# Kernel optimization log

Measured on AMD Instinct MI355X. Metric: run time of the kernel, lower is better.

Reference implementation:

```python
import jax, jax.numpy as jnp
import numpy as np

ALPHA = 1.0


def setup_inputs() -> dict:
    key = jax.random.key(0)
    ks = jax.random.split(key, 7)
    B, S, D_IN, D_OUT, R = 4, 2048, 2048, 2048, 64
    return {
        "x": jax.random.normal(ks[0], (B, S, D_IN), dtype=jnp.float32),
        "weight": jax.random.normal(ks[1], (D_OUT, D_IN), dtype=jnp.float32) * 0.02,
        "bias": jax.random.normal(ks[2], (D_OUT,), dtype=jnp.float32) * 0.02,
        "U": jax.random.normal(ks[3], (D_OUT, R), dtype=jnp.float32) * 0.02,
        "sigma": jax.random.normal(ks[4], (R, R), dtype=jnp.float32) * 0.02,
        "R": jax.random.normal(ks[5], (R, R), dtype=jnp.float32) * 0.02,
        "Vt": jax.random.normal(ks[6], (R, D_IN), dtype=jnp.float32) * 0.02,
    }


def reference(x, weight, bias, U, sigma, R, Vt):
    # base linear: F.linear(x, W, b) = x @ W^T + b
    base_out = jnp.einsum("bsi,oi->bso", x, weight) + bias
    # LoRA-XS delta: alpha * U @ sigma @ R @ Vt  -> [d_out, d_in]
    delta_W = ALPHA * (U @ sigma @ R @ Vt)
    lora_out = jnp.einsum("bsi,oi->bso", x, delta_W)
    return base_out + lora_out
```

## Files before the change

kernel.cpp:

```cpp
#include <hip/hip_runtime.h>
#include <hip/hip_bf16.h>
#include <stdint.h>

#define M_DIM 8192
#define K_DIM 2048
#define N_DIM 2048
#define RANK  64
#define ALPHA_F 1.0f

typedef __attribute__((ext_vector_type(4))) float  f32x4;
typedef __attribute__((ext_vector_type(8))) short  s16x8;

__device__ __forceinline__ unsigned short f2bf(float f) {
    unsigned int u = __float_as_uint(f);
    u += 0x7fffu + ((u >> 16) & 1u);
    return (unsigned short)(u >> 16);
}

__device__ __forceinline__ void gload_lds16(const void* g, void* l) {
    __builtin_amdgcn_global_load_lds(
        (const __attribute__((address_space(1))) void*)g,
        (__attribute__((address_space(3))) void*)l, 16, 0, 0);
}


__global__ __launch_bounds__(256) void t2sr_kernel(const float* __restrict__ sigma,
                                                   const float* __restrict__ Rm,
                                                   const float* __restrict__ Vt,
                                                   float* __restrict__ T2) {
    __shared__ float sSig[64];
    __shared__ float sRow[64];
    const int r = blockIdx.x >> 3;
    const int i = (blockIdx.x & 7) * 256 + threadIdx.x;
    if (threadIdx.x < 64) sSig[threadIdx.x] = sigma[r * 64 + threadIdx.x];
    __syncthreads();
    if (threadIdx.x < 64) {
        float a = 0.f;
        #pragma unroll 8
        for (int k = 0; k < 64; ++k) a += sSig[k] * Rm[k * 64 + threadIdx.x];
        sRow[threadIdx.x] = a;
    }
    __syncthreads();
    float a = 0.f;
    #pragma unroll 8
    for (int k = 0; k < 64; ++k) a += sRow[k] * Vt[k * 2048 + i];
    T2[r * 2048 + i] = a;
}

__global__ __launch_bounds__(256) void weffcast_kernel(const float* __restrict__ W,
                                                       const float* __restrict__ U,
                                                       const float* __restrict__ T2,
                                                       unsigned short* __restrict__ Wb,
                                                       const float* __restrict__ x,
                                                       unsigned short* __restrict__ xb) {
    __shared__ float sU[64 * 65];
    __shared__ float sT[64 * 64];
    if (blockIdx.x < 1024) {
        int to = blockIdx.x >> 5;
        int ti = blockIdx.x & 31;
        int o0 = to * 64, i0 = ti * 64;
        for (int e = 0; e < 16; ++e) {
            int li = threadIdx.x + e * 256;
            int hi = li >> 6, lo = li & 63;
            sU[hi * 65 + lo] = U[(size_t)o0 * 64 + li];
            sT[li]           = T2[hi * 2048 + i0 + lo];
        }
        __syncthreads();
        int o  = threadIdx.x >> 2;
        int ib = (threadIdx.x & 3) * 16;
        float acc[16] = {};
        for (int k = 0; k < 64; ++k) {
            float u = sU[o * 65 + k];
            #pragma unroll
            for (int j = 0; j < 16; ++j) acc[j] += u * sT[k * 64 + ib + j];
        }
        size_t base = (size_t)(o0 + o) * 2048 + i0 + ib;
        #pragma unroll
        for (int j = 0; j < 16; ++j)
            Wb[base + j] = f2bf(W[base + j] + ALPHA_F * acc[j]);
    } else {
        int cb = blockIdx.x - 1024;
        #pragma unroll
        for (int rep = 0; rep < 4; ++rep) {
            size_t idx = (((size_t)cb * 4 + rep) * 256 + threadIdx.x) * 8;
            f32x4 a = *reinterpret_cast<const f32x4*>(x + idx);
            f32x4 b = *reinterpret_cast<const f32x4*>(x + idx + 4);
            s16x8 o;
            o[0] = (short)f2bf(a[0]); o[1] = (short)f2bf(a[1]);
            o[2] = (short)f2bf(a[2]); o[3] = (short)f2bf(a[3]);
            o[4] = (short)f2bf(b[0]); o[5] = (short)f2bf(b[1]);
            o[6] = (short)f2bf(b[2]); o[7] = (short)f2bf(b[3]);
            *reinterpret_cast<s16x8*>(xb + idx) = o;
        }
    }
}


#define AHALF_E (128 * K_DIM)

__device__ __forceinline__ void stage_slot(const unsigned short* g0, const unsigned short* g1,
                                           char* smp, int ldsbase, int wave) {
    gload_lds16(g0, smp + ldsbase + wave * 1024);
    gload_lds16(g1, smp + ldsbase + 8192 + wave * 1024);
}

template <int B_, int P_>
__device__ __forceinline__ void read_a4(const char* sm, s16x8 (&af)[4], int wr8, int laneoff) {
    constexpr int ks = P_ & 1, mh = P_ >> 1;
    #pragma unroll
    for (int mi = 0; mi < 4; ++mi)
        af[mi] = *(const s16x8*)(sm + B_ * 32768 +
                    ((wr8 + mh * 4 + mi) * 2 + ks) * 1024 + laneoff);
}

template <int B_, int P_>
__device__ __forceinline__ void read_b4(const char* sm, s16x8 (&bfr4)[4][2], int wc4, int laneoff) {
    constexpr int ks = P_ & 1;
    #pragma unroll
    for (int ni = 0; ni < 4; ++ni)
        bfr4[ni][ks] = *(const s16x8*)(sm + 65536 + B_ * 32768 +
                          ((wc4 + ni) * 2 + ks) * 1024 + laneoff);
}

template <int P_>
__device__ __forceinline__ void mfma_p(f32x4 (&acc)[8][4], s16x8 (&af)[4], s16x8 (&bfr4)[4][2]) {
    constexpr int ks = P_ & 1, mh = P_ >> 1;
    #pragma unroll
    for (int mi = 0; mi < 4; ++mi)
        #pragma unroll
        for (int ni = 0; ni < 4; ++ni)
            acc[mh * 4 + mi][ni] = __builtin_amdgcn_mfma_f32_16x16x32_bf16(
                af[mi], bfr4[ni][ks], acc[mh * 4 + mi][ni], 0, 0, 0);
}

#define VMWAIT2 do { asm volatile("s_waitcnt vmcnt(2)" ::: "memory"); \
                     __builtin_amdgcn_sched_barrier(0); } while (0)
#define VMWAIT4 do { asm volatile("s_waitcnt vmcnt(4)" ::: "memory"); \
                     __builtin_amdgcn_sched_barrier(0); } while (0)

#define DO_PHASE(B_, P_, STAGE_STMT, WAIT_STMT)                         \
  { s16x8 af[4];                                                        \
    read_a4<B_, P_>(sm, af, wr8, laneoff);                              \
    if (P_ < 2) read_b4<B_, P_>(sm, bfr4, wc4, laneoff);                \
    STAGE_STMT;                                                         \
    WAIT_STMT;                                                          \
    __builtin_amdgcn_s_barrier();                                       \
    asm volatile("s_waitcnt lgkmcnt(0)" ::: "memory");                  \
    __builtin_amdgcn_sched_barrier(0);                                  \
    __builtin_amdgcn_s_setprio(1);                                      \
    mfma_p<P_>(acc, af, bfr4);                                          \
    __builtin_amdgcn_s_setprio(0); }

#define STAGE_A(half, buf, kel) \
    stage_slot(Ag + (half) * AHALF_E + (kel) + soff0, Ag + (half) * AHALF_E + (kel) + soff1, \
               sm, (buf) * 32768 + (half) * 16384, wave)
#define STAGE_B(half, buf, kel) \
    stage_slot(Bg + (half) * AHALF_E + (kel) + soff0, Bg + (half) * AHALF_E + (kel) + soff1, \
               sm, 65536 + (buf) * 32768 + (half) * 16384, wave)

__global__ __launch_bounds__(512, 2)
void gemm8_kernel(const unsigned short* __restrict__ A,
                  const unsigned short* __restrict__ Bm,
                  const float* __restrict__ bias,
                  float* __restrict__ C) {
    extern __shared__ char sm[];

    const int tid  = threadIdx.x;
    const int wave = tid >> 6;
    const int lane = tid & 63;
    const int wr8  = (wave >> 2) * 8;
    const int wc4  = (wave & 3) * 4;

    const int bid = blockIdx.x;
    const int swz = (bid & 7) * 32 + (bid >> 3);
    const int rowM0 = (swz >> 3) * 256;
    const int rowN0 = (swz & 7) * 256;

    const unsigned short* Ag = A  + (size_t)rowM0 * K_DIM;
    const unsigned short* Bg = Bm + (size_t)rowN0 * K_DIM;

    int soff0, soff1;
    {
        #pragma unroll
        for (int ld = 0; ld < 2; ++ld) {
            int D   = ld * 8192 + tid * 16;
            int st  = D >> 10;
            int s   = (D >> 4) & 63;
            int row = s >> 2;
            int kq  = (s & 3) ^ ((s >> 3) & 3);
            int e = ((st >> 1) * 16 + row) * K_DIM + (st & 1) * 32 + kq * 8;
            if (ld == 0) soff0 = e; else soff1 = e;
        }
    }

    const int laneoff = ((lane & 15) * 4 + ((lane >> 4) ^ (((lane & 15) >> 1) & 3))) * 16;

    f32x4 acc[8][4] = {};
    s16x8 bfr4[4][2];

    STAGE_A(0, 0, 0);
    STAGE_A(1, 0, 0);
    STAGE_B(0, 0, 0);
    STAGE_B(1, 0, 0);
    STAGE_B(0, 1, 64);
    STAGE_B(1, 1, 64);
    VMWAIT4;
    __builtin_amdgcn_s_barrier();

    for (int i = 0; i < 16; ++i) {
        const int kA12 = (2 * i + 1) * 64;
        const int kN2  = ((2 * i + 2) & 31) * 64;
        const int kN3  = ((2 * i + 3) & 31) * 64;

        DO_PHASE(0, 0, STAGE_A(0, 1, kA12), ((void)0));
        DO_PHASE(0, 1, STAGE_A(1, 1, kA12), ((void)0));
        DO_PHASE(0, 2, ((void)0),           ((void)0));
        DO_PHASE(0, 3, STAGE_B(0, 0, kN2),  VMWAIT2);
        DO_PHASE(1, 0, STAGE_B(1, 0, kN2),  ((void)0));
        DO_PHASE(1, 1, STAGE_A(0, 0, kN2),  ((void)0));
        DO_PHASE(1, 2, STAGE_A(1, 0, kN2),  ((void)0));
        DO_PHASE(1, 3, (STAGE_B(0, 1, kN3), STAGE_B(1, 1, kN3)), VMWAIT4);
    }

    const int col0  = rowN0 + (wc4 >> 2) * 64 + (lane & 15);
    const int row0w = rowM0 + (wr8 >> 3) * 128 + (lane >> 4) * 4;
    float bv[4];
    #pragma unroll
    for (int ni = 0; ni < 4; ++ni) bv[ni] = bias[col0 + ni * 16];
    #pragma unroll
    for (int mi = 0; mi < 8; ++mi)
        #pragma unroll
        for (int ni = 0; ni < 4; ++ni)
            #pragma unroll
            for (int r = 0; r < 4; ++r)
                C[(size_t)(row0w + mi * 16 + r) * N_DIM + col0 + ni * 16] =
                    acc[mi][ni][r] + bv[ni];
}


__global__ __launch_bounds__(256) void xt_kernel(const float* __restrict__ x,
                                                 const float* __restrict__ T2,
                                                 float* __restrict__ xt) {
    int idx = blockIdx.x * 256 + threadIdx.x;
    int m = idx >> 6, r = idx & 63;
    float acc = 0.f;
    for (int i = 0; i < K_DIM; ++i) acc += x[(size_t)m * K_DIM + i] * T2[r * K_DIM + i];
    xt[idx] = acc;
}

__global__ __launch_bounds__(256) void fgemm_kernel(const float* __restrict__ A,
                                                    const float* __restrict__ W,
                                                    const float* __restrict__ xt,
                                                    const float* __restrict__ U,
                                                    const float* __restrict__ bias,
                                                    float* __restrict__ C) {
    __shared__ float sA[64][17];
    __shared__ float sW[64][17];
    int bm = blockIdx.x >> 5;
    int bn = blockIdx.x & 31;
    int m0 = bm * 64, n0 = bn * 64;
    int tid = threadIdx.x;
    int tm = tid >> 4, tn = tid & 15;
    float acc[4][4] = {};
    for (int k0 = 0; k0 < K_DIM; k0 += 16) {
        int lr = tid >> 2;
        int lc = (tid & 3) * 4;
        #pragma unroll
        for (int j = 0; j < 4; ++j) {
            sA[lr][lc + j] = A[(size_t)(m0 + lr) * K_DIM + k0 + lc + j];
            sW[lr][lc + j] = W[(size_t)(n0 + lr) * K_DIM + k0 + lc + j];
        }
        __syncthreads();
        #pragma unroll
        for (int kk = 0; kk < 16; ++kk) {
            float av[4], wv[4];
            #pragma unroll
            for (int i = 0; i < 4; ++i) av[i] = sA[tm * 4 + i][kk];
            #pragma unroll
            for (int j = 0; j < 4; ++j) wv[j] = sW[tn * 4 + j][kk];
            #pragma unroll
            for (int i = 0; i < 4; ++i)
                #pragma unroll
                for (int j = 0; j < 4; ++j) acc[i][j] += av[i] * wv[j];
        }
        __syncthreads();
    }
    #pragma unroll
    for (int i = 0; i < 4; ++i) {
        int m = m0 + tm * 4 + i;
        #pragma unroll
        for (int j = 0; j < 4; ++j) {
            int n = n0 + tn * 4 + j;
            float l = 0.f;
            for (int r = 0; r < RANK; ++r) l += xt[(size_t)m * RANK + r] * U[(size_t)n * RANK + r];
            C[(size_t)m * N_DIM + n] = acc[i][j] + l + bias[n];
        }
    }
}

extern "C" void kernel_launch(void* const* d_in, const int* in_sizes, int n_in,
                              void* d_out, int out_size, void* d_ws, size_t ws_size,
                              hipStream_t stream) {
    const float* x      = (const float*)d_in[0];
    const float* weight = (const float*)d_in[1];
    const float* bias   = (const float*)d_in[2];
    const float* U      = (const float*)d_in[3];
    const float* sigma  = (const float*)d_in[4];
    const float* Rm     = (const float*)d_in[5];
    const float* Vt     = (const float*)d_in[6];
    float* out = (float*)d_out;
    char* ws = (char*)d_ws;

    const size_t XB_BYTES = (size_t)M_DIM * K_DIM * 2;
    const size_t WB_BYTES = (size_t)N_DIM * K_DIM * 2;
    const size_t T2_BYTES = (size_t)RANK * K_DIM * 4;
    const size_t MAIN_NEED = XB_BYTES + WB_BYTES + T2_BYTES;

    if (ws_size >= MAIN_NEED) {
        unsigned short* xb = (unsigned short*)ws;
        unsigned short* wb = (unsigned short*)(ws + XB_BYTES);
        float* T2 = (float*)(ws + XB_BYTES + WB_BYTES);

        hipFuncSetAttribute((const void*)gemm8_kernel,
                            hipFuncAttributeMaxDynamicSharedMemorySize, 131072);

        t2sr_kernel<<<512, 256, 0, stream>>>(sigma, Rm, Vt, T2);
        weffcast_kernel<<<3072, 256, 0, stream>>>(weight, U, T2, wb, x, xb);
        gemm8_kernel<<<(M_DIM / 256) * (N_DIM / 256), 512, 131072, stream>>>(xb, wb, bias, out);
    } else {
        float* T2 = (float*)ws;
        float* xt = (float*)(ws + T2_BYTES);
        t2sr_kernel<<<512, 256, 0, stream>>>(sigma, Rm, Vt, T2);
        xt_kernel<<<(M_DIM * RANK) / 256, 256, 0, stream>>>(x, T2, xt);
        fgemm_kernel<<<(M_DIM / 64) * (N_DIM / 64), 256, 0, stream>>>(x, weight, xt, U, bias, out);
    }
}
```

Before: 93.78 us.

## Software-pipeline LDS fragment reads ahead of MFMA with double-buffered A fragments

```diff
diff --git a/kernel.cpp b/kernel.cpp
--- a/kernel.cpp
+++ b/kernel.cpp
@@ -138,17 +138,15 @@
 #define VMWAIT4 do { asm volatile("s_waitcnt vmcnt(4)" ::: "memory"); \
                      __builtin_amdgcn_sched_barrier(0); } while (0)
 
-#define DO_PHASE(B_, P_, STAGE_STMT, WAIT_STMT)                         \
-  { s16x8 af[4];                                                        \
-    read_a4<B_, P_>(sm, af, wr8, laneoff);                              \
-    if (P_ < 2) read_b4<B_, P_>(sm, bfr4, wc4, laneoff);                \
-    STAGE_STMT;                                                         \
+#define DO_PHASE(P_CONSUME_B, P_CONSUME_P, AFC, NEXTREAD_STMT, NWAIT_LIT, STAGE_STMT, WAIT_STMT) \
+  { STAGE_STMT;                                                         \
     WAIT_STMT;                                                          \
     __builtin_amdgcn_s_barrier();                                       \
-    asm volatile("s_waitcnt lgkmcnt(0)" ::: "memory");                  \
+    NEXTREAD_STMT;                                                      \
+    asm volatile("s_waitcnt lgkmcnt(" NWAIT_LIT ")" ::: "memory");      \
     __builtin_amdgcn_sched_barrier(0);                                  \
     __builtin_amdgcn_s_setprio(1);                                      \
-    mfma_p<P_>(acc, af, bfr4);                                          \
+    mfma_p<P_CONSUME_P>(acc, AFC, bfr4);                                \
     __builtin_amdgcn_s_setprio(0); }
 
 #define STAGE_A(half, buf, kel) \
@@ -196,6 +194,7 @@
     const int laneoff = ((lane & 15) * 4 + ((lane >> 4) ^ (((lane & 15) >> 1) & 3))) * 16;
 
     f32x4 acc[8][4] = {};
+    s16x8 afA[4], afB[4];
     s16x8 bfr4[4][2];
 
     STAGE_A(0, 0, 0);
@@ -206,20 +205,42 @@
     STAGE_B(1, 1, 64);
     VMWAIT4;
     __builtin_amdgcn_s_barrier();
+    read_a4<0, 0>(sm, afA, wr8, laneoff);
+    read_b4<0, 0>(sm, bfr4, wc4, laneoff);
 
     for (int i = 0; i < 16; ++i) {
         const int kA12 = (2 * i + 1) * 64;
         const int kN2  = ((2 * i + 2) & 31) * 64;
         const int kN3  = ((2 * i + 3) & 31) * 64;
 
-        DO_PHASE(0, 0, STAGE_A(0, 1, kA12), ((void)0));
-        DO_PHASE(0, 1, STAGE_A(1, 1, kA12), ((void)0));
-        DO_PHASE(0, 2, ((void)0),           ((void)0));
-        DO_PHASE(0, 3, STAGE_B(0, 0, kN2),  VMWAIT2);
-        DO_PHASE(1, 0, STAGE_B(1, 0, kN2),  ((void)0));
-        DO_PHASE(1, 1, STAGE_A(0, 0, kN2),  ((void)0));
-        DO_PHASE(1, 2, STAGE_A(1, 0, kN2),  ((void)0));
-        DO_PHASE(1, 3, (STAGE_B(0, 1, kN3), STAGE_B(1, 1, kN3)), VMWAIT4);
+        DO_PHASE(0, 0, afA,
+                 (read_a4<0, 1>(sm, afB, wr8, laneoff),
+                  read_b4<0, 1>(sm, bfr4, wc4, laneoff)), "8",
+                 STAGE_A(0, 1, kA12), ((void)0));
+        DO_PHASE(0, 1, afB,
+                 (read_a4<0, 2>(sm, afA, wr8, laneoff)), "4",
+                 STAGE_A(1, 1, kA12), ((void)0));
+        DO_PHASE(0, 2, afA,
+                 (read_a4<0, 3>(sm, afB, wr8, laneoff)), "4",
+                 ((void)0), ((void)0));
+        DO_PHASE(0, 3, afB,
+                 (read_a4<1, 0>(sm, afA, wr8, laneoff),
+                  read_b4<1, 0>(sm, bfr4, wc4, laneoff)), "8",
+                 STAGE_B(0, 0, kN2), VMWAIT2);
+        DO_PHASE(1, 0, afA,
+                 (read_a4<1, 1>(sm, afB, wr8, laneoff),
+                  read_b4<1, 1>(sm, bfr4, wc4, laneoff)), "8",
+                 STAGE_B(1, 0, kN2), ((void)0));
+        DO_PHASE(1, 1, afB,
+                 (read_a4<1, 2>(sm, afA, wr8, laneoff)), "4",
+                 STAGE_A(0, 0, kN2), ((void)0));
+        DO_PHASE(1, 2, afA,
+                 (read_a4<1, 3>(sm, afB, wr8, laneoff)), "4",
+                 STAGE_A(1, 0, kN2), ((void)0));
+        DO_PHASE(1, 3, afB,
+                 (read_a4<0, 0>(sm, afA, wr8, laneoff),
+                  read_b4<0, 0>(sm, bfr4, wc4, laneoff)), "8",
+                 (STAGE_B(0, 1, kN3), STAGE_B(1, 1, kN3)), VMWAIT4);
     }
 
     const int col0  = rowN0 + (wc4 >> 2) * 64 + (lane & 15);
```

New measurement: 94.87 us. No clear change (+1.2%).

## Retile GEMM to 256x128 blocks with 4 waves and triple-buffered K=32 stages

Applied to the files above, without the earlier changes.

```diff
diff --git a/kernel.cpp b/kernel.cpp
--- a/kernel.cpp
+++ b/kernel.cpp
@@ -96,69 +96,93 @@
 }
 
 
-#define AHALF_E (128 * K_DIM)
-
-__device__ __forceinline__ void stage_slot(const unsigned short* g0, const unsigned short* g1,
-                                           char* smp, int ldsbase, int wave) {
-    gload_lds16(g0, smp + ldsbase + wave * 1024);
-    gload_lds16(g1, smp + ldsbase + 8192 + wave * 1024);
-}
-
-template <int B_, int P_>
-__device__ __forceinline__ void read_a4(const char* sm, s16x8 (&af)[4], int wr8, int laneoff) {
-    constexpr int ks = P_ & 1, mh = P_ >> 1;
+#define BUF0 0
+#define BUF1 24576
+#define BUF2 49152
+
+__device__ __forceinline__ void stage_a(const unsigned short* Ag, int kel, char* sm,
+                                        int tgt, int wave, int soff) {
+    #pragma unroll
+    for (int j = 0; j < 4; ++j) {
+        int s = wave * 4 + j;
+        gload_lds16(Ag + kel + s * 32768 + soff, sm + tgt + s * 1024);
+    }
+}
+__device__ __forceinline__ void stage_b(const unsigned short* Bg, int kel, char* sm,
+                                        int tgt, int wave, int soff) {
+    #pragma unroll
+    for (int j = 0; j < 2; ++j) {
+        int s = wave * 2 + j;
+        gload_lds16(Bg + kel + s * 32768 + soff, sm + tgt + 16384 + s * 1024);
+    }
+}
+
+template <int MH>
+__device__ __forceinline__ void read_a4(const char* sm, int cbuf, s16x8 (&af)[4],
+                                        int wrA8, int laneoff) {
     #pragma unroll
     for (int mi = 0; mi < 4; ++mi)
-        af[mi] = *(const s16x8*)(sm + B_ * 32768 +
-                    ((wr8 + mh * 4 + mi) * 2 + ks) * 1024 + laneoff);
-}
-
-template <int B_, int P_>
-__device__ __forceinline__ void read_b4(const char* sm, s16x8 (&bfr4)[4][2], int wc4, int laneoff) {
-    constexpr int ks = P_ & 1;
+        af[mi] = *(const s16x8*)(sm + cbuf + (wrA8 + MH * 4 + mi) * 1024 + laneoff);
+}
+__device__ __forceinline__ void read_b4(const char* sm, int cbuf, s16x8 (&bfr)[4],
+                                        int wcB4, int laneoff) {
     #pragma unroll
     for (int ni = 0; ni < 4; ++ni)
-        bfr4[ni][ks] = *(const s16x8*)(sm + 65536 + B_ * 32768 +
-                          ((wc4 + ni) * 2 + ks) * 1024 + laneoff);
-}
-
-template <int P_>
-__device__ __forceinline__ void mfma_p(f32x4 (&acc)[8][4], s16x8 (&af)[4], s16x8 (&bfr4)[4][2]) {
-    constexpr int ks = P_ & 1, mh = P_ >> 1;
+        bfr[ni] = *(const s16x8*)(sm + cbuf + 16384 + (wcB4 + ni) * 1024 + laneoff);
+}
+
+template <int MH>
+__device__ __forceinline__ void mfma16(f32x4 (&acc)[8][4], s16x8 (&af)[4], s16x8 (&bfr)[4]) {
     #pragma unroll
     for (int mi = 0; mi < 4; ++mi)
         #pragma unroll
         for (int ni = 0; ni < 4; ++ni)
-            acc[mh * 4 + mi][ni] = __builtin_amdgcn_mfma_f32_16x16x32_bf16(
-                af[mi], bfr4[ni][ks], acc[mh * 4 + mi][ni], 0, 0, 0);
-}
-
-#define VMWAIT2 do { asm volatile("s_waitcnt vmcnt(2)" ::: "memory"); \
+            acc[MH * 4 + mi][ni] = __builtin_amdgcn_mfma_f32_16x16x32_bf16(
+                af[mi], bfr[ni], acc[MH * 4 + mi][ni], 0, 0, 0);
+}
+
+#define VMWAIT6 do { asm volatile("s_waitcnt vmcnt(6)" ::: "memory"); \
                      __builtin_amdgcn_sched_barrier(0); } while (0)
-#define VMWAIT4 do { asm volatile("s_waitcnt vmcnt(4)" ::: "memory"); \
-                     __builtin_amdgcn_sched_barrier(0); } while (0)
-
-#define DO_PHASE(B_, P_, STAGE_STMT, WAIT_STMT)                         \
-  { s16x8 af[4];                                                        \
-    read_a4<B_, P_>(sm, af, wr8, laneoff);                              \
-    if (P_ < 2) read_b4<B_, P_>(sm, bfr4, wc4, laneoff);                \
-    STAGE_STMT;                                                         \
-    WAIT_STMT;                                                          \
-    __builtin_amdgcn_s_barrier();                                       \
-    asm volatile("s_waitcnt lgkmcnt(0)" ::: "memory");                  \
-    __builtin_amdgcn_sched_barrier(0);                                  \
-    __builtin_amdgcn_s_setprio(1);                                      \
-    mfma_p<P_>(acc, af, bfr4);                                          \
+
+#define PH_TAIL                                                  \
+    __builtin_amdgcn_s_barrier();                                \
+    asm volatile("s_waitcnt lgkmcnt(0)" ::: "memory");           \
+    __builtin_amdgcn_sched_barrier(0);                           \
+    __builtin_amdgcn_s_setprio(1);
+
+#define PHA(CBUF, TBUF, KEL)                                     \
+  { s16x8 af[4];                                                 \
+    read_a4<0>(sm, CBUF, af, wrA8, laneoff);                     \
+    read_b4(sm, CBUF, bfr, wcB4, laneoff);                       \
+    stage_a(Ag, (KEL), sm, TBUF, wave, soff);                    \
+    PH_TAIL                                                      \
+    mfma16<0>(acc, af, bfr);                                     \
     __builtin_amdgcn_s_setprio(0); }
 
-#define STAGE_A(half, buf, kel) \
-    stage_slot(Ag + (half) * AHALF_E + (kel) + soff0, Ag + (half) * AHALF_E + (kel) + soff1, \
-               sm, (buf) * 32768 + (half) * 16384, wave)
-#define STAGE_B(half, buf, kel) \
-    stage_slot(Bg + (half) * AHALF_E + (kel) + soff0, Bg + (half) * AHALF_E + (kel) + soff1, \
-               sm, 65536 + (buf) * 32768 + (half) * 16384, wave)
-
-__global__ __launch_bounds__(512, 2)
+#define PHB(CBUF, TBUF, KEL)                                     \
+  { s16x8 af[4];                                                 \
+    read_a4<1>(sm, CBUF, af, wrA8, laneoff);                     \
+    stage_b(Bg, (KEL), sm, TBUF, wave, soff);                    \
+    VMWAIT6;                                                     \
+    PH_TAIL                                                      \
+    mfma16<1>(acc, af, bfr);                                     \
+    __builtin_amdgcn_s_setprio(0); }
+
+#define PHA_NS(CBUF)                                             \
+  { s16x8 af[4];                                                 \
+    read_a4<0>(sm, CBUF, af, wrA8, laneoff);                     \
+    read_b4(sm, CBUF, bfr, wcB4, laneoff);                       \
+    PH_TAIL                                                      \
+    mfma16<0>(acc, af, bfr);                                     \
+    __builtin_amdgcn_s_setprio(0); }
+#define PHB_NS(CBUF)                                             \
+  { s16x8 af[4];                                                 \
+    read_a4<1>(sm, CBUF, af, wrA8, laneoff);                     \
+    PH_TAIL                                                      \
+    mfma16<1>(acc, af, bfr);                                     \
+    __builtin_amdgcn_s_setprio(0); }
+
+__global__ __launch_bounds__(256, 2)
 void gemm8_kernel(const unsigned short* __restrict__ A,
                   const unsigned short* __restrict__ Bm,
                   const float* __restrict__ bias,
@@ -168,62 +192,46 @@
     const int tid  = threadIdx.x;
     const int wave = tid >> 6;
     const int lane = tid & 63;
-    const int wr8  = (wave >> 2) * 8;
-    const int wc4  = (wave & 3) * 4;
+    const int wrA8 = (wave >> 1) * 8;
+    const int wcB4 = (wave & 1) * 4;
 
     const int bid = blockIdx.x;
-    const int swz = (bid & 7) * 32 + (bid >> 3);
-    const int rowM0 = (swz >> 3) * 256;
-    const int rowN0 = (swz & 7) * 256;
+    const int swz = (bid & 7) * 64 + (bid >> 3);
+    const int rowM0 = (swz >> 4) * 256;
+    const int rowN0 = (swz & 15) * 128;
 
     const unsigned short* Ag = A  + (size_t)rowM0 * K_DIM;
     const unsigned short* Bg = Bm + (size_t)rowN0 * K_DIM;
 
-    int soff0, soff1;
-    {
-        #pragma unroll
-        for (int ld = 0; ld < 2; ++ld) {
-            int D   = ld * 8192 + tid * 16;
-            int st  = D >> 10;
-            int s   = (D >> 4) & 63;
-            int row = s >> 2;
-            int kq  = (s & 3) ^ ((s >> 3) & 3);
-            int e = ((st >> 1) * 16 + row) * K_DIM + (st & 1) * 32 + kq * 8;
-            if (ld == 0) soff0 = e; else soff1 = e;
-        }
-    }
+    const int soff = (lane >> 2) * K_DIM + ((lane & 3) ^ ((lane >> 3) & 3)) * 8;
 
     const int laneoff = ((lane & 15) * 4 + ((lane >> 4) ^ (((lane & 15) >> 1) & 3))) * 16;
 
     f32x4 acc[8][4] = {};
-    s16x8 bfr4[4][2];
-
-    STAGE_A(0, 0, 0);
-    STAGE_A(1, 0, 0);
-    STAGE_B(0, 0, 0);
-    STAGE_B(1, 0, 0);
-    STAGE_B(0, 1, 64);
-    STAGE_B(1, 1, 64);
-    VMWAIT4;
+    s16x8 bfr[4];
+
+    stage_a(Ag, 0, sm, BUF0, wave, soff);
+    stage_b(Bg, 0, sm, BUF0, wave, soff);
+    stage_a(Ag, 32, sm, BUF1, wave, soff);
+    stage_b(Bg, 32, sm, BUF1, wave, soff);
+    VMWAIT6;
     __builtin_amdgcn_s_barrier();
 
-    for (int i = 0; i < 16; ++i) {
-        const int kA12 = (2 * i + 1) * 64;
-        const int kN2  = ((2 * i + 2) & 31) * 64;
-        const int kN3  = ((2 * i + 3) & 31) * 64;
-
-        DO_PHASE(0, 0, STAGE_A(0, 1, kA12), ((void)0));
-        DO_PHASE(0, 1, STAGE_A(1, 1, kA12), ((void)0));
-        DO_PHASE(0, 2, ((void)0),           ((void)0));
-        DO_PHASE(0, 3, STAGE_B(0, 0, kN2),  VMWAIT2);
-        DO_PHASE(1, 0, STAGE_B(1, 0, kN2),  ((void)0));
-        DO_PHASE(1, 1, STAGE_A(0, 0, kN2),  ((void)0));
-        DO_PHASE(1, 2, STAGE_A(1, 0, kN2),  ((void)0));
-        DO_PHASE(1, 3, (STAGE_B(0, 1, kN3), STAGE_B(1, 1, kN3)), VMWAIT4);
-    }
-
-    const int col0  = rowN0 + (wc4 >> 2) * 64 + (lane & 15);
-    const int row0w = rowM0 + (wr8 >> 3) * 128 + (lane >> 4) * 4;
+    for (int i = 0; i < 21; ++i) {
+        const int k2 = (3 * i + 2) * 32;
+        const int k3 = (3 * i + 3) * 32;
+        const int k4 = ((3 * i + 4) & 63) * 32;
+
+        PHA(BUF0, BUF2, k2); PHB(BUF0, BUF2, k2);
+        PHA(BUF1, BUF0, k3); PHB(BUF1, BUF0, k3);
+        PHA(BUF2, BUF1, k4); PHB(BUF2, BUF1, k4);
+    }
+    PHA_NS(BUF0); PHB_NS(BUF0);
+
+    asm volatile("s_waitcnt vmcnt(0)" ::: "memory");
+
+    const int col0  = rowN0 + (wave & 1) * 64 + (lane & 15);
+    const int row0w = rowM0 + (wave >> 1) * 128 + (lane >> 4) * 4;
     float bv[4];
     #pragma unroll
     for (int ni = 0; ni < 4; ++ni) bv[ni] = bias[col0 + ni * 16];
@@ -322,11 +330,11 @@
         float* T2 = (float*)(ws + XB_BYTES + WB_BYTES);
 
         hipFuncSetAttribute((const void*)gemm8_kernel,
-                            hipFuncAttributeMaxDynamicSharedMemorySize, 131072);
+                            hipFuncAttributeMaxDynamicSharedMemorySize, 73728);
 
         t2sr_kernel<<<512, 256, 0, stream>>>(sigma, Rm, Vt, T2);
         weffcast_kernel<<<3072, 256, 0, stream>>>(weight, U, T2, wb, x, xb);
-        gemm8_kernel<<<(M_DIM / 256) * (N_DIM / 256), 512, 131072, stream>>>(xb, wb, bias, out);
+        gemm8_kernel<<<(M_DIM / 256) * (N_DIM / 128), 256, 73728, stream>>>(xb, wb, bias, out);
     } else {
         float* T2 = (float*)ws;
         float* xt = (float*)(ws + T2_BYTES);
```

Result: slower. 103.4 us (+10.3%).
